# Kernel optimization log

Measured on AMD Instinct MI355X. Metric: run time of the kernel, lower is better.

The kernel has to match this reference:

```python
import jax, jax.numpy as jnp
import numpy as np

B, T, D = 2, 2048, 2048
N, K, H = 16, 8, 128            # heads, kv heads, head_dim
SOFT_CAP = 50.0
WINDOW = 1024
SCALE = H ** -0.5               # query_pre_attn_scalar
ROPE_BASE = 10000.0
ROPE_SCALE = 1.0
K_MASK = -2.3819763e+38


def rms_norm(x, scale, eps=1e-6):
    var = jnp.mean(jnp.square(x), axis=-1, keepdims=True)
    return x * jax.lax.rsqrt(var + eps) * (1.0 + scale)


def apply_rope(x, positions):
    # x: [B,T,heads,H]; positions: [B,T] int
    head_dim = x.shape[-1]
    fraction = 2.0 * jnp.arange(head_dim // 2, dtype=jnp.float32) / head_dim
    timescale = ROPE_BASE ** fraction                      # [H/2]
    sinusoid = positions[..., None].astype(jnp.float32) / timescale  # [B,T,H/2]
    sinusoid = sinusoid[..., None, :] / ROPE_SCALE          # [B,T,1,H/2]
    sin, cos = jnp.sin(sinusoid), jnp.cos(sinusoid)
    first, second = jnp.split(x, 2, axis=-1)
    return jnp.concatenate([first * cos - second * sin,
                            second * cos + first * sin], axis=-1)


def setup_inputs() -> dict:
    key = jax.random.key(0)
    ks = jax.random.split(key, 6)
    x = jax.random.normal(ks[0], (B, T, D), jnp.float32)
    q_w = jax.random.normal(ks[1], (N, D, H), jnp.float32) * (D ** -0.5)
    kv_w = jax.random.normal(ks[2], (2, K, D, H), jnp.float32) * (D ** -0.5)
    o_w = jax.random.normal(ks[3], (N, H, D), jnp.float32) * ((N * H) ** -0.5)
    qnorm_scale = 0.1 * jax.random.normal(ks[4], (H,), jnp.float32)
    knorm_scale = 0.1 * jax.random.normal(ks[5], (H,), jnp.float32)
    segment_pos = jnp.broadcast_to(jnp.arange(T, dtype=jnp.int32), (B, T))
    attn_mask = jnp.broadcast_to(jnp.tril(jnp.ones((T, T), dtype=bool)), (B, T, T))
    return {"x": x, "q_w": q_w, "kv_w": kv_w, "o_w": o_w,
            "qnorm_scale": qnorm_scale, "knorm_scale": knorm_scale,
            "segment_pos": segment_pos, "attn_mask": attn_mask}


def reference(x, q_w, kv_w, o_w, qnorm_scale, knorm_scale, segment_pos, attn_mask):
    # projections
    q = jnp.einsum('BTD,NDH->BTNH', x, q_w)            # [B,T,N,H]
    k = jnp.einsum('BSD,KDH->BSKH', x, kv_w[0])        # [B,T,K,H]
    v = jnp.einsum('BSD,KDH->BSKH', x, kv_w[1])
    # QK RMSNorm, then RoPE, then query scaling (matches source order)
    q = apply_rope(rms_norm(q, qnorm_scale), segment_pos) * SCALE
    k = apply_rope(rms_norm(k, knorm_scale), segment_pos)
    # GQA: regroup query heads per kv head
    G = N // K
    qg = q.reshape(B, T, K, G, H)
    logits = jnp.einsum('BTKGH,BSKH->BTKGS', qg, k).reshape(B, T, N, T)
    # logit soft cap
    logits = jnp.tanh(logits / SOFT_CAP) * SOFT_CAP
    # sliding window mask combined with causal attn_mask
    pos_q = segment_pos[:, :, None]
    pos_k = segment_pos[:, None, :]
    sliding = (pos_k > pos_q - WINDOW) & (pos_k < pos_q + WINDOW)
    mask = attn_mask & sliding                          # [B,T,S]
    padded = jnp.where(mask[:, :, None, :], logits, K_MASK)
    probs = jax.nn.softmax(padded, axis=-1).astype(k.dtype)
    enc = jnp.einsum('BTKGS,BSKH->BTKGH',
                     probs.reshape(B, T, K, G, T), v).reshape(B, T, N, H)
    return jnp.einsum('BTNH,NHD->BTD', enc, o_w)
```

## Files before the change

### kernel.cpp

```cpp
#include <hip/hip_runtime.h>
#include <stdint.h>

#define BB 2
#define TT 2048
#define DD 2048
#define NHD 16
#define KVH 8
#define HD 128
#define JC 4096
#define WIN 1024
#define SCALE_Q 0.08838834764831845f

typedef __attribute__((ext_vector_type(8))) short bf16x8;
typedef __attribute__((ext_vector_type(8))) unsigned short us8;
typedef __attribute__((ext_vector_type(4))) unsigned short us4;
typedef __attribute__((ext_vector_type(4))) float f32x4;
typedef __attribute__((ext_vector_type(16))) float f32x16;
typedef __attribute__((ext_vector_type(4))) unsigned int u32x4;

#define GAS __attribute__((address_space(1)))
#define LAS __attribute__((address_space(3)))

__device__ __forceinline__ unsigned short f2bf(float f) {
  unsigned u = __float_as_uint(f);
  u += 0x7FFFu + ((u >> 16) & 1u);
  return (unsigned short)(u >> 16);
}
__device__ __forceinline__ float bf2f(unsigned short u) {
  return __uint_as_float(((unsigned)u) << 16);
}

__device__ __forceinline__ void gload16(const void* g, void* l) {
  __builtin_amdgcn_global_load_lds((const GAS unsigned int*)g, (LAS unsigned int*)l, 16, 0, 0);
}

#define VMCNT(n) asm volatile("s_waitcnt vmcnt(" #n ")" ::: "memory")

__global__ void __launch_bounds__(256) k_cvt(const float4* __restrict__ in,
                                             us4* __restrict__ out, int n4) {
  int i = blockIdx.x * 256 + threadIdx.x;
  if (i >= n4) return;
  float4 v = in[i];
  us4 o;
  o[0] = f2bf(v.x); o[1] = f2bf(v.y); o[2] = f2bf(v.z); o[3] = f2bf(v.w);
  out[i] = o;
}

__global__ void __launch_bounds__(256) k_transpose_cvt(
    const float* __restrict__ in, unsigned short* __restrict__ out,
    int R, int C, int ldin, long b0s, int nbi, long b1s, long obs) {
  __shared__ float tile[32][33];
  int z = blockIdx.z;
  const float* ib = in + (long)(z / nbi) * b0s + (long)(z % nbi) * b1s;
  unsigned short* ob = out + (long)z * obs;
  int c0 = blockIdx.x * 32, r0 = blockIdx.y * 32;
  int tx = threadIdx.x, ty = threadIdx.y;
#pragma unroll
  for (int i = 0; i < 4; i++)
    tile[ty + i * 8][tx] = ib[(long)(r0 + ty + i * 8) * ldin + c0 + tx];
  __syncthreads();
#pragma unroll
  for (int i = 0; i < 4; i++)
    ob[(long)(c0 + ty + i * 8) * R + r0 + tx] = f2bf(tile[tx][ty + i * 8]);
}

__global__ void __launch_bounds__(256) k_wt(const float* __restrict__ qw,
                                            const float* __restrict__ kvw,
                                            unsigned short* __restrict__ out) {
  __shared__ float tile[32][33];
  int z = blockIdx.z;
  const float* ib = (z < 16) ? qw + (long)z * 2048 * 128 : kvw + (long)(z - 16) * 2048 * 128;
  unsigned short* ob = out + (long)z * 128 * 2048;
  int c0 = blockIdx.x * 32, r0 = blockIdx.y * 32;
  int tx = threadIdx.x, ty = threadIdx.y;
#pragma unroll
  for (int i = 0; i < 4; i++)
    tile[ty + i * 8][tx] = ib[(long)(r0 + ty + i * 8) * 128 + c0 + tx];
  __syncthreads();
#pragma unroll
  for (int i = 0; i < 4; i++)
    ob[(long)(c0 + ty + i * 8) * 2048 + r0 + tx] = f2bf(tile[tx][ty + i * 8]);
}

__global__ void __launch_bounds__(256) k_transpose_bf(
    const unsigned short* __restrict__ in, unsigned short* __restrict__ out,
    int R, int C, int ldin, long b0s, int nbi, long b1s, long obs) {
  __shared__ unsigned short tile[32][33];
  int z = blockIdx.z;
  const unsigned short* ib = in + (long)(z / nbi) * b0s + (long)(z % nbi) * b1s;
  unsigned short* ob = out + (long)z * obs;
  int c0 = blockIdx.x * 32, r0 = blockIdx.y * 32;
  int tx = threadIdx.x, ty = threadIdx.y;
#pragma unroll
  for (int i = 0; i < 4; i++)
    tile[ty + i * 8][tx] = ib[(long)(r0 + ty + i * 8) * ldin + c0 + tx];
  __syncthreads();
#pragma unroll
  for (int i = 0; i < 4; i++)
    ob[(long)(c0 + ty + i * 8) * R + r0 + tx] = tile[tx][ty + i * 8];
}

template <int BM, int BN, int NWN, int THREADS, int NBUF, bool BF16OUT>
__global__ void __launch_bounds__(THREADS, 2) k_gemm9(
    const unsigned short* __restrict__ A, const unsigned short* __restrict__ Bt,
    void* __restrict__ Cv, int M, int Nn, int nby) {
  constexpr int KD = 2048;
  constexpr int NT = KD / 32;
  constexpr int ROWS = BM + BN;
  constexpr int RPI = THREADS / 4;
  constexpr int IA = BM / RPI;
  constexpr int IPT = ROWS / RPI;
  constexpr int MT = 8, MT2 = 4;
  __shared__ short lds[NBUF][ROWS * 32];

  int tid = threadIdx.x, lane = tid & 63, w = tid >> 6;
  int wm = w / NWN, wn = w % NWN;
  int id = blockIdx.x;
  int cpx = gridDim.x >> 3;
  id = (id & 7) * cpx + (id >> 3);
  int m0 = (id / nby) * BM, n0 = (id % nby) * BN;

  int srow = tid >> 2;
  int scol = ((tid & 3) ^ ((tid >> 3) & 3)) * 8;
  const unsigned short* gA = A + (long)(m0 + srow) * KD + scol;
  const unsigned short* gB = Bt + (long)(n0 + srow) * KD + scol;

  auto STG = [&](int p, int ko, int j) {
    if (j < IA)
      gload16(gA + (long)j * RPI * KD + ko, &lds[p][(j * RPI + w * 16) * 32]);
    else
      gload16(gB + (long)(j - IA) * RPI * KD + ko,
              &lds[p][(BM + (j - IA) * RPI + w * 16) * 32]);
  };

  int frag = (lane & 15) * 32 + (((lane >> 4) ^ ((lane >> 1) & 3)) * 8);
  int abase = wm * 128 * 32 + frag;
  int bbase = (BM + wn * 64) * 32 + frag;

  f32x4 acc[MT][4] = {};
#pragma unroll
  for (int tt = 0; tt < NBUF - 1; ++tt)
#pragma unroll
    for (int j = 0; j < IPT; ++j) STG(tt, tt * 32, j);
  if constexpr (IPT * (NBUF - 2) == 8) VMCNT(8);
  else VMCNT(6);
  __builtin_amdgcn_s_barrier();

  int buf = 0, sp = NBUF - 1;
  for (int t = 0; t < NT; ++t) {
    const short* bufp = lds[buf];
    bool st = (t + NBUF - 1) < NT;
    int ko = (t + NBUF - 1) * 32;
    bf16x8 bfr[4], af[MT2];
#pragma unroll
    for (int ni = 0; ni < 4; ++ni)
      bfr[ni] = *(const bf16x8*)&bufp[bbase + ni * 16 * 32];
#pragma unroll
    for (int mi = 0; mi < MT2; ++mi)
      af[mi] = *(const bf16x8*)&bufp[abase + mi * 16 * 32];
    if (st) {
#pragma unroll
      for (int j = 0; j < IPT / 2; ++j) STG(sp, ko, j);
    }
    __builtin_amdgcn_s_barrier();
    asm volatile("s_waitcnt lgkmcnt(0)" ::: "memory");
    __builtin_amdgcn_sched_barrier(0);
    __builtin_amdgcn_s_setprio(1);
#pragma unroll
    for (int mi = 0; mi < MT2; ++mi)
#pragma unroll
      for (int ni = 0; ni < 4; ++ni)
        acc[mi][ni] = __builtin_amdgcn_mfma_f32_16x16x32_bf16(af[mi], bfr[ni], acc[mi][ni], 0, 0, 0);
    __builtin_amdgcn_s_setprio(0);
    __builtin_amdgcn_s_barrier();
    bf16x8 af2[MT2];
#pragma unroll
    for (int mi = 0; mi < MT2; ++mi)
      af2[mi] = *(const bf16x8*)&bufp[abase + (MT2 + mi) * 16 * 32];
    if (st) {
#pragma unroll
      for (int j = IPT / 2; j < IPT; ++j) STG(sp, ko, j);
    }
    {
      int rem = NT - 2 - t;
      if (rem > NBUF - 2) rem = NBUF - 2;
      if (rem == 2) {
        if constexpr (IPT == 4) VMCNT(8); else VMCNT(12);
      } else if (rem == 1) {
        if constexpr (IPT == 4) VMCNT(4); else VMCNT(6);
      } else if (rem == 0) {
        VMCNT(0);
      }
    }
    __builtin_amdgcn_s_barrier();
    asm volatile("s_waitcnt lgkmcnt(0)" ::: "memory");
    __builtin_amdgcn_sched_barrier(0);
    __builtin_amdgcn_s_setprio(1);
#pragma unroll
    for (int mi = 0; mi < MT2; ++mi)
#pragma unroll
      for (int ni = 0; ni < 4; ++ni)
        acc[MT2 + mi][ni] = __builtin_amdgcn_mfma_f32_16x16x32_bf16(af2[mi], bfr[ni], acc[MT2 + mi][ni], 0, 0, 0);
    __builtin_amdgcn_s_setprio(0);
    __builtin_amdgcn_s_barrier();
    buf = (buf == NBUF - 1) ? 0 : buf + 1;
    sp = (sp == NBUF - 1) ? 0 : sp + 1;
  }

#pragma unroll
  for (int mi = 0; mi < MT; mi++)
#pragma unroll
    for (int ni = 0; ni < 4; ni++)
#pragma unroll
      for (int r = 0; r < 4; r++) {
        int row = m0 + wm * 128 + mi * 16 + (lane >> 4) * 4 + r;
        int col = n0 + wn * 64 + ni * 16 + (lane & 15);
        if constexpr (BF16OUT)
          ((unsigned short*)Cv)[(long)row * Nn + col] = f2bf(acc[mi][ni][r]);
        else
          ((float*)Cv)[(long)row * Nn + col] = acc[mi][ni][r];
      }
}

__global__ void __launch_bounds__(256) k_norm_rope(
    const unsigned short* __restrict__ qkv, const float* __restrict__ qns,
    const float* __restrict__ kns,
    unsigned short* __restrict__ qb, unsigned short* __restrict__ kb) {
  int wid = threadIdx.x >> 6, lane = threadIdx.x & 63;
  long r = (long)blockIdx.x * 4 + wid;
  int b = (int)(r / (TT * 24));
  int rem = (int)(r % (TT * 24));
  int t = rem / 24, hd = rem % 24;
  const unsigned short* row = qkv + (long)(b * TT + t) * JC + (hd < 16 ? hd * HD : 2048 + (hd - 16) * HD);
  float f0 = bf2f(row[lane]), f1 = bf2f(row[lane + 64]);
  float ss = f0 * f0 + f1 * f1;
#pragma unroll
  for (int m = 1; m < 64; m <<= 1) ss += __shfl_xor(ss, m, 64);
  float rinv = rsqrtf(ss * (1.0f / 128.0f) + 1e-6f);
  const float* sc = (hd < 16) ? qns : kns;
  float y0 = f0 * rinv * (1.0f + sc[lane]);
  float y1 = f1 * rinv * (1.0f + sc[lane + 64]);
  float ts = exp2f((float)lane * (13.287712379549449f / 64.0f));
  float ang = (float)t / ts;
  float s, c;
  sincosf(ang, &s, &c);
  float o0 = y0 * c - y1 * s;
  float o1 = y1 * c + y0 * s;
  unsigned short* dst;
  if (hd < 16) {
    o0 *= SCALE_Q; o1 *= SCALE_Q;
    dst = qb + ((long)(b * NHD + hd) * TT + t) * HD;
  } else {
    dst = kb + ((long)(b * KVH + (hd - 16)) * TT + t) * HD;
  }
  dst[lane] = f2bf(o0);
  dst[lane + 64] = f2bf(o1);
}

template <bool FULL>
__device__ __forceinline__ void softcap16(const f32x16& s16, float* pr, float& lsum,
                                          int s_base, int tq, int g) {
#pragma unroll
  for (int r = 0; r < 16; r++) {
    float x = s16[r];
    float e = __builtin_amdgcn_exp2f(-0.05770780163555853f * fabsf(x));
    float u = (x > 0.0f ? e : 1.0f) * __builtin_amdgcn_rcpf(1.0f + e);
    float p = __builtin_amdgcn_exp2f(-144.26950408889634f * u);
    if (!FULL) {
      int s = s_base + (r & 3) + 8 * (r >> 2) + 4 * g;
      bool valid = (s <= tq) && (s > tq - WIN);
      p = valid ? p : 0.0f;
    }
    lsum += p;
    pr[r] = p;
  }
}

__device__ __forceinline__ void hswap(unsigned& a, unsigned& b, int g) {
  unsigned ax = (unsigned)__shfl_xor((int)a, 32, 64);
  unsigned bx = (unsigned)__shfl_xor((int)b, 32, 64);
  unsigned r0 = g ? bx : a;
  unsigned r1 = g ? b : ax;
  a = r0; b = r1;
}

__global__ void __launch_bounds__(256, 1) k_attn(
    const unsigned short* __restrict__ qb, const unsigned short* __restrict__ kb,
    const unsigned short* __restrict__ vbT, unsigned short* __restrict__ enc) {
  __shared__ short Kl[2][64][128];
  __shared__ short Vt[2][128][64];
  int tid = threadIdx.x, lane = tid & 63, w = tid >> 6;
  int g = lane >> 5, l31 = lane & 31;
  int id = blockIdx.x;
  int b = id >> 7;
  int rem = id & 127;
  int n = rem >> 3;
  int ti = rem & 7;
  int t0 = ti * 256;
  int kh = n >> 1;
  const unsigned short* qbase = qb + ((long)(b * NHD + n) * TT + t0 + w * 64) * HD;
  const unsigned short* kbase = kb + (long)(b * KVH + kh) * TT * HD;
  const unsigned short* vbase = vbT + (long)(b * KVH + kh) * HD * TT;

  bf16x8 bq[2][8];
#pragma unroll
  for (int qg = 0; qg < 2; qg++) {
    const unsigned short* qp = qbase + (long)(qg * 32 + l31) * HD + g * 8;
#pragma unroll
    for (int kb8 = 0; kb8 < 8; kb8++)
      bq[qg][kb8] = *(const bf16x8*)(qp + kb8 * 16);
  }

  f32x16 acc0[4] = {}, acc1[4] = {};
  float lsum0 = 0.0f, lsum1 = 0.0f;
  int t0w = t0 + w * 64;
  int s_begin = (t0 >= WIN) ? t0 - WIN : 0;
  int s_end = t0 + 256;

  auto STAGE = [&](int buf, int s0) {
#pragma unroll
    for (int i = 0; i < 4; i++) {
      int row = w * 16 + i * 4 + (lane >> 4);
      int c16 = (lane & 15) ^ (row & 7);
      gload16(kbase + (long)(s0 + row) * HD + c16 * 8, &Kl[buf][w * 16 + i * 4][0]);
    }
#pragma unroll
    for (int i = 0; i < 4; i++) {
      int row = w * 32 + i * 8 + (lane >> 3);
      int c16 = (lane & 7) ^ (row & 7);
      gload16(vbase + (long)row * TT + s0 + c16 * 8, &Vt[buf][w * 32 + i * 8][0]);
    }
  };

  auto PROC = [&](const f32x16& sv, int qg, float& ls, unsigned (*pwp)[4], int sb, int s0) {
    int base = t0w + qg * 32;
    int tq = base + l31;
    float pr[16];
    bool fullg = (s0 + 63 <= base) && (s0 >= base + 32 - WIN);
    if (fullg) softcap16<true>(sv, pr, ls, 0, tq, g);
    else       softcap16<false>(sv, pr, ls, s0 + sb * 32, tq, g);
    unsigned X[4], Y[4];
#pragma unroll
    for (int m = 0; m < 4; m++) {
      asm("v_cvt_pk_bf16_f32 %0, %1, %2" : "=v"(X[m]) : "v"(pr[4 * m]), "v"(pr[4 * m + 1]));
      asm("v_cvt_pk_bf16_f32 %0, %1, %2" : "=v"(Y[m]) : "v"(pr[4 * m + 2]), "v"(pr[4 * m + 3]));
    }
#pragma unroll
    for (int kl = 0; kl < 2; kl++) {
      hswap(X[2 * kl], X[2 * kl + 1], g);
      hswap(Y[2 * kl], Y[2 * kl + 1], g);
      pwp[sb * 2 + kl][0] = X[2 * kl];
      pwp[sb * 2 + kl][1] = Y[2 * kl];
      pwp[sb * 2 + kl][2] = X[2 * kl + 1];
      pwp[sb * 2 + kl][3] = Y[2 * kl + 1];
    }
  };

  STAGE(0, s_begin);
  __syncthreads();
  int cur = 0;
  for (int s0 = s_begin; s0 < s_end; s0 += 64) {
    if (s0 + 64 < s_end) STAGE(cur ^ 1, s0 + 64);
    bool live = (s0 <= t0w + 63) && (s0 + 63 >= t0w - (WIN - 1));
    if (live) {
      unsigned pw0[4][4], pw1[4][4];
#pragma unroll
      for (int sb = 0; sb < 2; sb++) {
        int srow = sb * 32 + l31;
        f32x16 s0v = {}, s1v = {};
#pragma unroll
        for (int kb8 = 0; kb8 < 8; kb8++) {
          bf16x8 ak = *(const bf16x8*)&Kl[cur][srow][8 * ((2 * kb8 + g) ^ (srow & 7))];
          s0v = __builtin_amdgcn_mfma_f32_32x32x16_bf16(ak, bq[0][kb8], s0v, 0, 0, 0);
          s1v = __builtin_amdgcn_mfma_f32_32x32x16_bf16(ak, bq[1][kb8], s1v, 0, 0, 0);
        }
        PROC(s0v, 0, lsum0, pw0, sb, s0);
        PROC(s1v, 1, lsum1, pw1, sb, s0);
      }
#pragma unroll
      for (int ks = 0; ks < 4; ks++) {
        u32x4 t40 = {pw0[ks][0], pw0[ks][1], pw0[ks][2], pw0[ks][3]};
        u32x4 t41 = {pw1[ks][0], pw1[ks][1], pw1[ks][2], pw1[ks][3]};
        bf16x8 pb0 = __builtin_bit_cast(bf16x8, t40);
        bf16x8 pb1 = __builtin_bit_cast(bf16x8, t41);
#pragma unroll
        for (int ht = 0; ht < 4; ht++) {
          int hrow = ht * 32 + l31;
          bf16x8 av = *(const bf16x8*)&Vt[cur][hrow][8 * ((2 * ks + g) ^ (hrow & 7))];
          acc0[ht] = __builtin_amdgcn_mfma_f32_32x32x16_bf16(av, pb0, acc0[ht], 0, 0, 0);
          acc1[ht] = __builtin_amdgcn_mfma_f32_32x32x16_bf16(av, pb1, acc1[ht], 0, 0, 0);
        }
      }
    }
    __syncthreads();
    cur ^= 1;
  }

  lsum0 += __shfl_xor(lsum0, 32, 64);
  lsum1 += __shfl_xor(lsum1, 32, 64);
  float inv0 = __builtin_amdgcn_rcpf(lsum0);
  float inv1 = __builtin_amdgcn_rcpf(lsum1);
  unsigned short* dst0 = enc + ((long)(b * TT + t0w + l31) * NHD + n) * HD;
  unsigned short* dst1 = enc + ((long)(b * TT + t0w + 32 + l31) * NHD + n) * HD;
#pragma unroll
  for (int ht = 0; ht < 4; ht++)
#pragma unroll
    for (int r4 = 0; r4 < 4; r4++) {
      us4 o0, o1;
#pragma unroll
      for (int e = 0; e < 4; e++) {
        o0[e] = f2bf(acc0[ht][r4 * 4 + e] * inv0);
        o1[e] = f2bf(acc1[ht][r4 * 4 + e] * inv1);
      }
      *(us4*)(dst0 + ht * 32 + 8 * r4 + 4 * g) = o0;
      *(us4*)(dst1 + ht * 32 + 8 * r4 + 4 * g) = o1;
    }
}

extern "C" void kernel_launch(void* const* d_in, const int* in_sizes, int n_in,
                              void* d_out, int out_size, void* d_ws, size_t ws_size,
                              hipStream_t stream) {
  const float* x    = (const float*)d_in[0];
  const float* q_w  = (const float*)d_in[1];
  const float* kv_w = (const float*)d_in[2];
  const float* o_w  = (const float*)d_in[3];
  const float* qns  = (const float*)d_in[4];
  const float* kns  = (const float*)d_in[5];

  if (ws_size < (104ull << 20)) return;
  char* ws = (char*)d_ws;
  unsigned short* qkvb = (unsigned short*)(ws + 0);
  unsigned short* enc  = (unsigned short*)(ws + 0);
  unsigned short* x_bf = (unsigned short*)(ws + (64ll << 20));
  unsigned short* qb   = (unsigned short*)(ws + (64ll << 20));
  unsigned short* Wt   = (unsigned short*)(ws + (80ll << 20));
  unsigned short* kb   = (unsigned short*)(ws + (80ll << 20));
  unsigned short* vbT  = (unsigned short*)(ws + (88ll << 20));
  unsigned short* Wt_o = (unsigned short*)(ws + (96ll << 20));

  dim3 tb(32, 8, 1);
  k_cvt<<<8192, 256, 0, stream>>>((const float4*)x, (us4*)x_bf, 2097152);
  k_wt<<<dim3(4, 64, 32), tb, 0, stream>>>(q_w, kv_w, Wt);
  k_transpose_cvt<<<dim3(64, 64, 1), tb, 0, stream>>>(o_w, Wt_o, 2048, 2048, 2048, 0, 1, 0, 0);
  k_gemm9<256, 256, 4, 512, 4, true><<<256, 512, 0, stream>>>(x_bf, Wt, qkvb, 4096, 4096, 16);
  k_transpose_bf<<<dim3(4, 64, 16), tb, 0, stream>>>(qkvb + 3072, vbT, 2048, 128, 4096,
                                                     (long)2048 * 4096, 8, 128, (long)128 * 2048);
  k_norm_rope<<<24576, 256, 0, stream>>>(qkvb, qns, kns, qb, kb);
  k_attn<<<256, 256, 0, stream>>>(qb, kb, vbT, enc);
  k_gemm9<256, 128, 2, 256, 3, false><<<256, 256, 0, stream>>>(enc, Wt_o, (float*)d_out, 4096, 2048, 16);
}
```

Measured before the change: 250.5 us.

## Halve attention query tile to 128 rows, double grid and occupancy

```diff
diff --git a/kernel.cpp b/kernel.cpp
--- a/kernel.cpp
+++ b/kernel.cpp
@@ -284,7 +284,7 @@
   a = r0; b = r1;
 }
 
-__global__ void __launch_bounds__(256, 1) k_attn(
+__global__ void __launch_bounds__(256, 2) k_attn(
     const unsigned short* __restrict__ qb, const unsigned short* __restrict__ kb,
     const unsigned short* __restrict__ vbT, unsigned short* __restrict__ enc) {
   __shared__ short Kl[2][64][128];
@@ -292,30 +292,31 @@
   int tid = threadIdx.x, lane = tid & 63, w = tid >> 6;
   int g = lane >> 5, l31 = lane & 31;
   int id = blockIdx.x;
-  int b = id >> 7;
-  int rem = id & 127;
-  int n = rem >> 3;
-  int ti = rem & 7;
-  int t0 = ti * 256;
+  int b = id >> 8;
+  int rem = id & 255;
+  int n = rem >> 4;
+  int traw = rem & 15;
+  int tile = b ? ((traw + 8) & 15) : traw;
+  int t0 = tile * 128;
   int kh = n >> 1;
-  const unsigned short* qbase = qb + ((long)(b * NHD + n) * TT + t0 + w * 64) * HD;
+  const unsigned short* qbase = qb + ((long)(b * NHD + n) * TT + t0 + w * 32) * HD;
   const unsigned short* kbase = kb + (long)(b * KVH + kh) * TT * HD;
   const unsigned short* vbase = vbT + (long)(b * KVH + kh) * HD * TT;
 
-  bf16x8 bq[2][8];
-#pragma unroll
-  for (int qg = 0; qg < 2; qg++) {
-    const unsigned short* qp = qbase + (long)(qg * 32 + l31) * HD + g * 8;
+  bf16x8 bq[8];
+  {
+    const unsigned short* qp = qbase + (long)l31 * HD + g * 8;
 #pragma unroll
     for (int kb8 = 0; kb8 < 8; kb8++)
-      bq[qg][kb8] = *(const bf16x8*)(qp + kb8 * 16);
+      bq[kb8] = *(const bf16x8*)(qp + kb8 * 16);
   }
 
-  f32x16 acc0[4] = {}, acc1[4] = {};
-  float lsum0 = 0.0f, lsum1 = 0.0f;
-  int t0w = t0 + w * 64;
+  f32x16 acc[4] = {};
+  float lsum = 0.0f;
+  int t0w = t0 + w * 32;
+  int tq = t0w + l31;
   int s_begin = (t0 >= WIN) ? t0 - WIN : 0;
-  int s_end = t0 + 256;
+  int s_end = t0 + 128;
 
   auto STAGE = [&](int buf, int s0) {
 #pragma unroll
@@ -329,30 +330,6 @@
       int row = w * 32 + i * 8 + (lane >> 3);
       int c16 = (lane & 7) ^ (row & 7);
       gload16(vbase + (long)row * TT + s0 + c16 * 8, &Vt[buf][w * 32 + i * 8][0]);
-    }
-  };
-
-  auto PROC = [&](const f32x16& sv, int qg, float& ls, unsigned (*pwp)[4], int sb, int s0) {
-    int base = t0w + qg * 32;
-    int tq = base + l31;
-    float pr[16];
-    bool fullg = (s0 + 63 <= base) && (s0 >= base + 32 - WIN);
-    if (fullg) softcap16<true>(sv, pr, ls, 0, tq, g);
-    else       softcap16<false>(sv, pr, ls, s0 + sb * 32, tq, g);
-    unsigned X[4], Y[4];
-#pragma unroll
-    for (int m = 0; m < 4; m++) {
-      asm("v_cvt_pk_bf16_f32 %0, %1, %2" : "=v"(X[m]) : "v"(pr[4 * m]), "v"(pr[4 * m + 1]));
-      asm("v_cvt_pk_bf16_f32 %0, %1, %2" : "=v"(Y[m]) : "v"(pr[4 * m + 2]), "v"(pr[4 * m + 3]));
-    }
-#pragma unroll
-    for (int kl = 0; kl < 2; kl++) {
-      hswap(X[2 * kl], X[2 * kl + 1], g);
-      hswap(Y[2 * kl], Y[2 * kl + 1], g);
-      pwp[sb * 2 + kl][0] = X[2 * kl];
-      pwp[sb * 2 + kl][1] = Y[2 * kl];
-      pwp[sb * 2 + kl][2] = X[2 * kl + 1];
-      pwp[sb * 2 + kl][3] = Y[2 * kl + 1];
     }
   };
 
@@ -361,34 +338,50 @@
   int cur = 0;
   for (int s0 = s_begin; s0 < s_end; s0 += 64) {
     if (s0 + 64 < s_end) STAGE(cur ^ 1, s0 + 64);
-    bool live = (s0 <= t0w + 63) && (s0 + 63 >= t0w - (WIN - 1));
+    bool live = (s0 <= t0w + 31) && (s0 + 63 >= t0w - (WIN - 1));
     if (live) {
-      unsigned pw0[4][4], pw1[4][4];
+      f32x16 sc2[2] = {};
 #pragma unroll
       for (int sb = 0; sb < 2; sb++) {
         int srow = sb * 32 + l31;
-        f32x16 s0v = {}, s1v = {};
 #pragma unroll
         for (int kb8 = 0; kb8 < 8; kb8++) {
           bf16x8 ak = *(const bf16x8*)&Kl[cur][srow][8 * ((2 * kb8 + g) ^ (srow & 7))];
-          s0v = __builtin_amdgcn_mfma_f32_32x32x16_bf16(ak, bq[0][kb8], s0v, 0, 0, 0);
-          s1v = __builtin_amdgcn_mfma_f32_32x32x16_bf16(ak, bq[1][kb8], s1v, 0, 0, 0);
+          sc2[sb] = __builtin_amdgcn_mfma_f32_32x32x16_bf16(ak, bq[kb8], sc2[sb], 0, 0, 0);
         }
-        PROC(s0v, 0, lsum0, pw0, sb, s0);
-        PROC(s1v, 1, lsum1, pw1, sb, s0);
       }
+      bool full = (s0 + 63 <= t0w) && (s0 >= t0w + 31 - (WIN - 1));
+      unsigned pw[4][4];
+#pragma unroll
+      for (int sb = 0; sb < 2; sb++) {
+        float pr[16];
+        if (full) softcap16<true>(sc2[sb], pr, lsum, 0, tq, g);
+        else      softcap16<false>(sc2[sb], pr, lsum, s0 + sb * 32, tq, g);
+        unsigned X[4], Y[4];
+#pragma unroll
+        for (int m = 0; m < 4; m++) {
+          asm("v_cvt_pk_bf16_f32 %0, %1, %2" : "=v"(X[m]) : "v"(pr[4 * m]), "v"(pr[4 * m + 1]));
+          asm("v_cvt_pk_bf16_f32 %0, %1, %2" : "=v"(Y[m]) : "v"(pr[4 * m + 2]), "v"(pr[4 * m + 3]));
+        }
+#pragma unroll
+        for (int kl = 0; kl < 2; kl++) {
+          hswap(X[2 * kl], X[2 * kl + 1], g);
+          hswap(Y[2 * kl], Y[2 * kl + 1], g);
+          pw[sb * 2 + kl][0] = X[2 * kl];
+          pw[sb * 2 + kl][1] = Y[2 * kl];
+          pw[sb * 2 + kl][2] = X[2 * kl + 1];
+          pw[sb * 2 + kl][3] = Y[2 * kl + 1];
+        }
+      }
 #pragma unroll
       for (int ks = 0; ks < 4; ks++) {
-        u32x4 t40 = {pw0[ks][0], pw0[ks][1], pw0[ks][2], pw0[ks][3]};
-        u32x4 t41 = {pw1[ks][0], pw1[ks][1], pw1[ks][2], pw1[ks][3]};
-        bf16x8 pb0 = __builtin_bit_cast(bf16x8, t40);
-        bf16x8 pb1 = __builtin_bit_cast(bf16x8, t41);
+        u32x4 t4 = {pw[ks][0], pw[ks][1], pw[ks][2], pw[ks][3]};
+        bf16x8 pb = __builtin_bit_cast(bf16x8, t4);
 #pragma unroll
         for (int ht = 0; ht < 4; ht++) {
           int hrow = ht * 32 + l31;
           bf16x8 av = *(const bf16x8*)&Vt[cur][hrow][8 * ((2 * ks + g) ^ (hrow & 7))];
-          acc0[ht] = __builtin_amdgcn_mfma_f32_32x32x16_bf16(av, pb0, acc0[ht], 0, 0, 0);
-          acc1[ht] = __builtin_amdgcn_mfma_f32_32x32x16_bf16(av, pb1, acc1[ht], 0, 0, 0);
+          acc[ht] = __builtin_amdgcn_mfma_f32_32x32x16_bf16(av, pb, acc[ht], 0, 0, 0);
         }
       }
     }
@@ -396,24 +389,17 @@
     cur ^= 1;
   }
 
-  lsum0 += __shfl_xor(lsum0, 32, 64);
-  lsum1 += __shfl_xor(lsum1, 32, 64);
-  float inv0 = __builtin_amdgcn_rcpf(lsum0);
-  float inv1 = __builtin_amdgcn_rcpf(lsum1);
-  unsigned short* dst0 = enc + ((long)(b * TT + t0w + l31) * NHD + n) * HD;
-  unsigned short* dst1 = enc + ((long)(b * TT + t0w + 32 + l31) * NHD + n) * HD;
+  lsum += __shfl_xor(lsum, 32, 64);
+  float inv = __builtin_amdgcn_rcpf(lsum);
+  unsigned short* dst = enc + ((long)(b * TT + tq) * NHD + n) * HD;
 #pragma unroll
   for (int ht = 0; ht < 4; ht++)
 #pragma unroll
     for (int r4 = 0; r4 < 4; r4++) {
-      us4 o0, o1;
-#pragma unroll
-      for (int e = 0; e < 4; e++) {
-        o0[e] = f2bf(acc0[ht][r4 * 4 + e] * inv0);
-        o1[e] = f2bf(acc1[ht][r4 * 4 + e] * inv1);
-      }
-      *(us4*)(dst0 + ht * 32 + 8 * r4 + 4 * g) = o0;
-      *(us4*)(dst1 + ht * 32 + 8 * r4 + 4 * g) = o1;
+      us4 o;
+#pragma unroll
+      for (int e = 0; e < 4; e++) o[e] = f2bf(acc[ht][r4 * 4 + e] * inv);
+      *(us4*)(dst + ht * 32 + 8 * r4 + 4 * g) = o;
     }
 }
 
@@ -446,6 +432,6 @@
   k_transpose_bf<<<dim3(4, 64, 16), tb, 0, stream>>>(qkvb + 3072, vbT, 2048, 128, 4096,
                                                      (long)2048 * 4096, 8, 128, (long)128 * 2048);
   k_norm_rope<<<24576, 256, 0, stream>>>(qkvb, qns, kns, qb, kb);
-  k_attn<<<256, 256, 0, stream>>>(qb, kb, vbT, enc);
+  k_attn<<<512, 256, 0, stream>>>(qb, kb, vbT, enc);
   k_gemm9<256, 128, 2, 256, 3, false><<<256, 256, 0, stream>>>(enc, Wt_o, (float*)d_out, 4096, 2048, 16);
 }
```

Result: faster. 224.9 us (-10.2%).

## Split attention KV range across two wave groups, merge weight prep kernels

Applied to the files above, without the earlier changes.

```diff
diff --git a/kernel.cpp b/kernel.cpp
--- a/kernel.cpp
+++ b/kernel.cpp
@@ -46,36 +46,30 @@
   out[i] = o;
 }
 
-__global__ void __launch_bounds__(256) k_transpose_cvt(
-    const float* __restrict__ in, unsigned short* __restrict__ out,
-    int R, int C, int ldin, long b0s, int nbi, long b1s, long obs) {
+__global__ void __launch_bounds__(256) k_prep(
+    const float* __restrict__ qw, const float* __restrict__ kvw,
+    const float* __restrict__ ow, unsigned short* __restrict__ Wt,
+    unsigned short* __restrict__ Wt_o) {
   __shared__ float tile[32][33];
-  int z = blockIdx.z;
-  const float* ib = in + (long)(z / nbi) * b0s + (long)(z % nbi) * b1s;
-  unsigned short* ob = out + (long)z * obs;
-  int c0 = blockIdx.x * 32, r0 = blockIdx.y * 32;
+  int id = blockIdx.x;
+  const float* ib;
+  unsigned short* ob;
+  int ldin, c0, r0;
+  if (id < 8192) {
+    int bx = id & 3, by = (id >> 2) & 63, z = id >> 8;
+    ib = (z < 16) ? qw + (long)z * 2048 * 128 : kvw + (long)(z - 16) * 2048 * 128;
+    ob = Wt + (long)z * 128 * 2048;
+    ldin = 128;
+    c0 = bx * 32; r0 = by * 32;
+  } else {
+    int t = id - 8192;
+    ib = ow; ob = Wt_o; ldin = 2048;
+    c0 = (t & 63) * 32; r0 = (t >> 6) * 32;
+  }
   int tx = threadIdx.x, ty = threadIdx.y;
 #pragma unroll
   for (int i = 0; i < 4; i++)
     tile[ty + i * 8][tx] = ib[(long)(r0 + ty + i * 8) * ldin + c0 + tx];
-  __syncthreads();
-#pragma unroll
-  for (int i = 0; i < 4; i++)
-    ob[(long)(c0 + ty + i * 8) * R + r0 + tx] = f2bf(tile[tx][ty + i * 8]);
-}
-
-__global__ void __launch_bounds__(256) k_wt(const float* __restrict__ qw,
-                                            const float* __restrict__ kvw,
-                                            unsigned short* __restrict__ out) {
-  __shared__ float tile[32][33];
-  int z = blockIdx.z;
-  const float* ib = (z < 16) ? qw + (long)z * 2048 * 128 : kvw + (long)(z - 16) * 2048 * 128;
-  unsigned short* ob = out + (long)z * 128 * 2048;
-  int c0 = blockIdx.x * 32, r0 = blockIdx.y * 32;
-  int tx = threadIdx.x, ty = threadIdx.y;
-#pragma unroll
-  for (int i = 0; i < 4; i++)
-    tile[ty + i * 8][tx] = ib[(long)(r0 + ty + i * 8) * 128 + c0 + tx];
   __syncthreads();
 #pragma unroll
   for (int i = 0; i < 4; i++)
@@ -263,9 +257,8 @@
 #pragma unroll
   for (int r = 0; r < 16; r++) {
     float x = s16[r];
-    float e = __builtin_amdgcn_exp2f(-0.05770780163555853f * fabsf(x));
-    float u = (x > 0.0f ? e : 1.0f) * __builtin_amdgcn_rcpf(1.0f + e);
-    float p = __builtin_amdgcn_exp2f(-144.26950408889634f * u);
+    float e2 = __builtin_amdgcn_exp2f(0.05770780163555853f * x);
+    float p = __builtin_amdgcn_exp2f(-144.26950408889634f * __builtin_amdgcn_rcpf(1.0f + e2));
     if (!FULL) {
       int s = s_base + (r & 3) + 8 * (r >> 2) + 4 * g;
       bool valid = (s <= tq) && (s > tq - WIN);
@@ -284,12 +277,14 @@
   a = r0; b = r1;
 }
 
-__global__ void __launch_bounds__(256, 1) k_attn(
+__global__ void __launch_bounds__(512, 1) k_attn(
     const unsigned short* __restrict__ qb, const unsigned short* __restrict__ kb,
     const unsigned short* __restrict__ vbT, unsigned short* __restrict__ enc) {
-  __shared__ short Kl[2][64][128];
-  __shared__ short Vt[2][128][64];
+  __shared__ char smem[133120];
+  short* Kl = (short*)smem;
+  short* Vt = (short*)(smem + 65536);
   int tid = threadIdx.x, lane = tid & 63, w = tid >> 6;
+  int G = w >> 2, wi = w & 3;
   int g = lane >> 5, l31 = lane & 31;
   int id = blockIdx.x;
   int b = id >> 7;
@@ -298,7 +293,8 @@
   int ti = rem & 7;
   int t0 = ti * 256;
   int kh = n >> 1;
-  const unsigned short* qbase = qb + ((long)(b * NHD + n) * TT + t0 + w * 64) * HD;
+  int qb0 = t0 + wi * 64;
+  const unsigned short* qbase = qb + ((long)(b * NHD + n) * TT + qb0) * HD;
   const unsigned short* kbase = kb + (long)(b * KVH + kh) * TT * HD;
   const unsigned short* vbase = vbT + (long)(b * KVH + kh) * HD * TT;
 
@@ -313,27 +309,29 @@
 
   f32x16 acc0[4] = {}, acc1[4] = {};
   float lsum0 = 0.0f, lsum1 = 0.0f;
-  int t0w = t0 + w * 64;
-  int s_begin = (t0 >= WIN) ? t0 - WIN : 0;
-  int s_end = t0 + 256;
+  int s_base = (t0 >= WIN) ? t0 - WIN : 0;
+  int NTg = ((t0 + 256 - s_base) >> 6) >> 1;
+  int gs0 = s_base + G * NTg * 64;
 
   auto STAGE = [&](int buf, int s0) {
+    short* Kb = Kl + (G * 2 + buf) * 8192;
+    short* Vb = Vt + (G * 2 + buf) * 8192;
 #pragma unroll
     for (int i = 0; i < 4; i++) {
-      int row = w * 16 + i * 4 + (lane >> 4);
+      int row = wi * 16 + i * 4 + (lane >> 4);
       int c16 = (lane & 15) ^ (row & 7);
-      gload16(kbase + (long)(s0 + row) * HD + c16 * 8, &Kl[buf][w * 16 + i * 4][0]);
+      gload16(kbase + (long)(s0 + row) * HD + c16 * 8, Kb + (wi * 16 + i * 4) * 128);
     }
 #pragma unroll
     for (int i = 0; i < 4; i++) {
-      int row = w * 32 + i * 8 + (lane >> 3);
+      int row = wi * 32 + i * 8 + (lane >> 3);
       int c16 = (lane & 7) ^ (row & 7);
-      gload16(vbase + (long)row * TT + s0 + c16 * 8, &Vt[buf][w * 32 + i * 8][0]);
+      gload16(vbase + (long)row * TT + s0 + c16 * 8, Vb + (wi * 32 + i * 8) * 64);
     }
   };
 
   auto PROC = [&](const f32x16& sv, int qg, float& ls, unsigned (*pwp)[4], int sb, int s0) {
-    int base = t0w + qg * 32;
+    int base = qb0 + qg * 32;
     int tq = base + l31;
     float pr[16];
     bool fullg = (s0 + 63 <= base) && (s0 >= base + 32 - WIN);
@@ -356,13 +354,16 @@
     }
   };
 
-  STAGE(0, s_begin);
+  STAGE(0, gs0);
   __syncthreads();
   int cur = 0;
-  for (int s0 = s_begin; s0 < s_end; s0 += 64) {
-    if (s0 + 64 < s_end) STAGE(cur ^ 1, s0 + 64);
-    bool live = (s0 <= t0w + 63) && (s0 + 63 >= t0w - (WIN - 1));
+  for (int it = 0; it < NTg; ++it) {
+    int s0 = gs0 + it * 64;
+    if (it + 1 < NTg) STAGE(cur ^ 1, s0 + 64);
+    bool live = (s0 <= qb0 + 63) && (s0 + 63 >= qb0 - (WIN - 1));
     if (live) {
+      const short* Kb = Kl + (G * 2 + cur) * 8192;
+      const short* Vb = Vt + (G * 2 + cur) * 8192;
       unsigned pw0[4][4], pw1[4][4];
 #pragma unroll
       for (int sb = 0; sb < 2; sb++) {
@@ -370,7 +371,7 @@
         f32x16 s0v = {}, s1v = {};
 #pragma unroll
         for (int kb8 = 0; kb8 < 8; kb8++) {
-          bf16x8 ak = *(const bf16x8*)&Kl[cur][srow][8 * ((2 * kb8 + g) ^ (srow & 7))];
+          bf16x8 ak = *(const bf16x8*)&Kb[srow * 128 + 8 * ((2 * kb8 + g) ^ (srow & 7))];
           s0v = __builtin_amdgcn_mfma_f32_32x32x16_bf16(ak, bq[0][kb8], s0v, 0, 0, 0);
           s1v = __builtin_amdgcn_mfma_f32_32x32x16_bf16(ak, bq[1][kb8], s1v, 0, 0, 0);
         }
@@ -386,7 +387,7 @@
 #pragma unroll
         for (int ht = 0; ht < 4; ht++) {
           int hrow = ht * 32 + l31;
-          bf16x8 av = *(const bf16x8*)&Vt[cur][hrow][8 * ((2 * ks + g) ^ (hrow & 7))];
+          bf16x8 av = *(const bf16x8*)&Vb[hrow * 64 + 8 * ((2 * ks + g) ^ (hrow & 7))];
           acc0[ht] = __builtin_amdgcn_mfma_f32_32x32x16_bf16(av, pb0, acc0[ht], 0, 0, 0);
           acc1[ht] = __builtin_amdgcn_mfma_f32_32x32x16_bf16(av, pb1, acc1[ht], 0, 0, 0);
         }
@@ -396,25 +397,54 @@
     cur ^= 1;
   }
 
-  lsum0 += __shfl_xor(lsum0, 32, 64);
-  lsum1 += __shfl_xor(lsum1, 32, 64);
-  float inv0 = __builtin_amdgcn_rcpf(lsum0);
-  float inv1 = __builtin_amdgcn_rcpf(lsum1);
-  unsigned short* dst0 = enc + ((long)(b * TT + t0w + l31) * NHD + n) * HD;
-  unsigned short* dst1 = enc + ((long)(b * TT + t0w + 32 + l31) * NHD + n) * HD;
-#pragma unroll
-  for (int ht = 0; ht < 4; ht++)
-#pragma unroll
-    for (int r4 = 0; r4 < 4; r4++) {
-      us4 o0, o1;
-#pragma unroll
-      for (int e = 0; e < 4; e++) {
-        o0[e] = f2bf(acc0[ht][r4 * 4 + e] * inv0);
-        o1[e] = f2bf(acc1[ht][r4 * 4 + e] * inv1);
+  float* accx = (float*)smem;
+  float* lsx = (float*)(smem + 131072);
+  if (G == 1) {
+#pragma unroll
+    for (int qg = 0; qg < 2; qg++) {
+      const f32x16* a = qg ? acc1 : acc0;
+#pragma unroll
+      for (int ht = 0; ht < 4; ht++)
+#pragma unroll
+        for (int e = 0; e < 16; e++)
+          accx[((((wi * 2 + qg) * 4 + ht) * 16) + e) * 64 + lane] = a[ht][e];
+    }
+    lsx[(wi * 2 + 0) * 64 + lane] = lsum0;
+    lsx[(wi * 2 + 1) * 64 + lane] = lsum1;
+  }
+  __syncthreads();
+  if (G == 0) {
+#pragma unroll
+    for (int qg = 0; qg < 2; qg++) {
+      f32x16* a = qg ? acc1 : acc0;
+#pragma unroll
+      for (int ht = 0; ht < 4; ht++)
+#pragma unroll
+        for (int e = 0; e < 16; e++)
+          a[ht][e] += accx[((((wi * 2 + qg) * 4 + ht) * 16) + e) * 64 + lane];
+    }
+    lsum0 += lsx[(wi * 2 + 0) * 64 + lane];
+    lsum1 += lsx[(wi * 2 + 1) * 64 + lane];
+    lsum0 += __shfl_xor(lsum0, 32, 64);
+    lsum1 += __shfl_xor(lsum1, 32, 64);
+    float inv0 = __builtin_amdgcn_rcpf(lsum0);
+    float inv1 = __builtin_amdgcn_rcpf(lsum1);
+    unsigned short* dst0 = enc + ((long)(b * TT + qb0 + l31) * NHD + n) * HD;
+    unsigned short* dst1 = enc + ((long)(b * TT + qb0 + 32 + l31) * NHD + n) * HD;
+#pragma unroll
+    for (int ht = 0; ht < 4; ht++)
+#pragma unroll
+      for (int r4 = 0; r4 < 4; r4++) {
+        us4 o0, o1;
+#pragma unroll
+        for (int e = 0; e < 4; e++) {
+          o0[e] = f2bf(acc0[ht][r4 * 4 + e] * inv0);
+          o1[e] = f2bf(acc1[ht][r4 * 4 + e] * inv1);
+        }
+        *(us4*)(dst0 + ht * 32 + 8 * r4 + 4 * g) = o0;
+        *(us4*)(dst1 + ht * 32 + 8 * r4 + 4 * g) = o1;
       }
-      *(us4*)(dst0 + ht * 32 + 8 * r4 + 4 * g) = o0;
-      *(us4*)(dst1 + ht * 32 + 8 * r4 + 4 * g) = o1;
-    }
+  }
 }
 
 extern "C" void kernel_launch(void* const* d_in, const int* in_sizes, int n_in,
@@ -440,12 +470,11 @@
 
   dim3 tb(32, 8, 1);
   k_cvt<<<8192, 256, 0, stream>>>((const float4*)x, (us4*)x_bf, 2097152);
-  k_wt<<<dim3(4, 64, 32), tb, 0, stream>>>(q_w, kv_w, Wt);
-  k_transpose_cvt<<<dim3(64, 64, 1), tb, 0, stream>>>(o_w, Wt_o, 2048, 2048, 2048, 0, 1, 0, 0);
+  k_prep<<<12288, tb, 0, stream>>>(q_w, kv_w, o_w, Wt, Wt_o);
   k_gemm9<256, 256, 4, 512, 4, true><<<256, 512, 0, stream>>>(x_bf, Wt, qkvb, 4096, 4096, 16);
   k_transpose_bf<<<dim3(4, 64, 16), tb, 0, stream>>>(qkvb + 3072, vbT, 2048, 128, 4096,
                                                      (long)2048 * 4096, 8, 128, (long)128 * 2048);
   k_norm_rope<<<24576, 256, 0, stream>>>(qkvb, qns, kns, qb, kb);
-  k_attn<<<256, 256, 0, stream>>>(qb, kb, vbT, enc);
+  k_attn<<<256, 512, 0, stream>>>(qb, kb, vbT, enc);
   k_gemm9<256, 128, 2, 256, 3, false><<<256, 256, 0, stream>>>(enc, Wt_o, (float*)d_out, 4096, 2048, 16);
 }
```

After: 290.1 us. +15.8%, slower.
